# Optimization experiments

Hardware: AMD Instinct MI355X
Metric: run time of the kernel (lower is better)

## Reference

```python
import jax, jax.numpy as jnp
import numpy as np

UPDATE_SCALE = 1.0
DIST_THRESHOLD = 3.0
W_INJECT = 1.0
W_PIXEL = 1.0
EPS = 1e-8
BIG = 1e6  # sentinel coordinate for masked-out gt points


def extract_zc(sdf):
    """Zero crossings along vertical then horizontal neighbor pairs.
    Returns pts [Ncand,2] float, mask [Ncand] bool (fixed-size, masked)."""
    H, W = sdf.shape
    ii = jnp.arange(H, dtype=sdf.dtype)
    jj = jnp.arange(W, dtype=sdf.dtype)
    # vertical pairs (i,j)-(i+1,j): shape [H-1, W]
    v1, v2 = sdf[:-1, :], sdf[1:, :]
    a = jnp.abs(v1) / (jnp.abs(v1) + jnp.abs(v2) + EPS)
    i0 = ii[:-1, None]
    rv = jnp.where(v1 == 0, i0, jnp.where(v2 == 0, i0 + 1.0, i0 + a))
    cv = jnp.broadcast_to(jj[None, :], v1.shape)
    mv = (v1 == 0) | (v2 == 0) | (v1 * v2 < 0)
    # horizontal pairs (i,j)-(i,j+1): shape [H, W-1]
    h1, h2 = sdf[:, :-1], sdf[:, 1:]
    b = jnp.abs(h1) / (jnp.abs(h1) + jnp.abs(h2) + EPS)
    j0 = jj[None, :-1]
    ch = jnp.where(h1 == 0, j0, jnp.where(h2 == 0, j0 + 1.0, j0 + b))
    rh = jnp.broadcast_to(ii[:, None], h1.shape)
    mh = (h1 == 0) | (h2 == 0) | (h1 * h2 < 0)
    pts = jnp.concatenate([
        jnp.stack([rv.ravel(), cv.ravel()], axis=1),
        jnp.stack([rh.ravel(), ch.ravel()], axis=1)], axis=0)
    mask = jnp.concatenate([mv.ravel(), mh.ravel()], axis=0)
    return pts, mask


def compute_normals(sdf):
    # central differences, one-sided at edges -> [H,W,2]
    gr = jnp.concatenate([sdf[1:2] - sdf[0:1], (sdf[2:] - sdf[:-2]) / 2.0,
                          sdf[-1:] - sdf[-2:-1]], axis=0)
    gc = jnp.concatenate([sdf[:, 1:2] - sdf[:, 0:1], (sdf[:, 2:] - sdf[:, :-2]) / 2.0,
                          sdf[:, -1:] - sdf[:, -2:-1]], axis=1)
    return jnp.stack([gr, gc], axis=2)


def _corners(pts, H, W):
    r, c = pts[:, 0], pts[:, 1]
    r0 = jnp.clip(jnp.floor(r).astype(jnp.int32), 0, H - 1)
    c0 = jnp.clip(jnp.floor(c).astype(jnp.int32), 0, W - 1)
    r1 = jnp.clip(r0 + 1, 0, H - 1)
    c1 = jnp.clip(c0 + 1, 0, W - 1)
    ar = r - r0.astype(r.dtype)
    ac = c - c0.astype(c.dtype)
    wa = (1 - ar) * (1 - ac); wb = (1 - ar) * ac
    wc = ar * (1 - ac); wd = ar * ac
    return r0, c0, r1, c1, wa, wb, wc, wd


def bilinear_gather(img, pts):
    H, W = img.shape[0], img.shape[1]
    r0, c0, r1, c1, wa, wb, wc, wd = _corners(pts, H, W)
    if img.ndim == 3:
        wa, wb, wc, wd = wa[:, None], wb[:, None], wc[:, None], wd[:, None]
    return (img[r0, c0] * wa + img[r0, c1] * wb
            + img[r1, c0] * wc + img[r1, c1] * wd)


def one_image(pred, gt):
    H, W = pred.shape
    gt_pts, gt_m = extract_zc(jax.lax.stop_gradient(gt))
    pr_pts, pr_m = extract_zc(jax.lax.stop_gradient(pred))
    # bilinearly sampled, normalized normals at pred zero crossings
    normals = compute_normals(pred)                         # [H,W,2]
    n = bilinear_gather(normals, pr_pts)                    # [M,2]
    n = n / (jnp.linalg.norm(n, axis=1, keepdims=True) + 1e-8)
    # brute-force NN of each pred ZC point in gt ZC points (masked gt -> far away)
    gp = jnp.where(gt_m[:, None], gt_pts, BIG)              # [N,2]
    d2 = ((pr_pts ** 2).sum(1)[:, None] + (gp ** 2).sum(1)[None, :]
          - 2.0 * pr_pts @ gp.T)                            # [M,N]
    d2 = jnp.maximum(d2, 0.0)
    idx = jnp.argmin(d2, axis=1)
    md2 = jnp.min(d2, axis=1)
    near = gp[idx]                                          # [M,2]
    contrib = pr_m & (md2 <= DIST_THRESHOLD ** 2)
    dirv = near - pr_pts
    dot = jnp.where(contrib, (dirv * n).sum(1) * UPDATE_SCALE, 0.0)
    # bilinear scatter of dot into dSDF (weights vanish exactly where torch skips out-of-range)
    r0, c0, r1, c1, wa, wb, wc, wd = _corners(pr_pts, H, W)
    dSDF = jnp.zeros_like(pred)
    dSDF = (dSDF.at[r0, c0].add(dot * wa)
                 .at[r0, c1].add(dot * wb)
                 .at[r1, c0].add(dot * wc)
                 .at[r1, c1].add(dot * wd))
    dSDF = jax.lax.stop_gradient(dSDF)
    inj = jnp.sum(pred * dSDF)
    vals = bilinear_gather(pred, pr_pts)                    # [M]
    pix = jnp.sum(jnp.where(pr_m, vals, 0.0))
    return inj, pix


def setup_inputs() -> dict:
    key = jax.random.key(0)
    k1, k2 = jax.random.split(key)
    B, H, W = 1, 96, 96
    pred_sdf = jax.random.normal(k1, (B, H, W), dtype=jnp.float32)
    gt_sdf = jax.random.normal(k2, (B, H, W), dtype=jnp.float32)
    return {"pred_sdf": pred_sdf, "gt_sdf": gt_sdf}


def reference(pred_sdf, gt_sdf):
    inj, pix = jax.vmap(one_image)(pred_sdf, gt_sdf)
    inject = inj.mean()
    pixel = pix.mean()
    return W_INJECT * inject + W_PIXEL * pixel
```

## Files before the change

kernel.cpp:

```cpp
#include <hip/hip_runtime.h>
#include <math.h>

#pragma clang fp contract(off)

#define HH 96
#define WW 96
#define NV 9120
#define NC 18240
#define NPIX 9216
#define NCELL 9216
#define SLOTS 4
#define NBLK2 1140
#define PBLK 72
#define BIGF 1000000.0f
#define SENT_D 3.4e38f
#define SENT_J 0x7fffffff

__global__ __launch_bounds__(256) void k_prep(
    const float* __restrict__ PR, const float* __restrict__ GT,
    float2* __restrict__ N2, float2* prP, int* prM,
    float4* cells, int* finCnt){
#pragma clang fp contract(off)
  int t = blockIdx.x*256 + threadIdx.x;
  if (t == 0) *finCnt = 0;
  if (t < NPIX){
    int i = t / WW, j = t % WW;
    float gr, gc;
    if (i == 0)         gr = PR[WW+j] - PR[j];
    else if (i == HH-1) gr = PR[(HH-1)*WW+j] - PR[(HH-2)*WW+j];
    else                gr = (PR[(i+1)*WW+j] - PR[(i-1)*WW+j]) / 2.0f;
    if (j == 0)         gc = PR[i*WW+1] - PR[i*WW];
    else if (j == WW-1) gc = PR[i*WW+WW-1] - PR[i*WW+WW-2];
    else                gc = (PR[i*WW+j+1] - PR[i*WW+j-1]) / 2.0f;
    N2[t] = make_float2(gr, gc);
    int cnt = 0;
    float4 slot[SLOTS];
    for (int s = 0; s < 2; ++s){
      int i0 = i - 1 + s;
      if (i0 >= 0 && i0 <= HH-2){
        float v1 = GT[i0*WW+j], v2 = GT[(i0+1)*WW+j];
        int m = (v1 == 0.0f) || (v2 == 0.0f) || ((v1*v2) < 0.0f);
        if (m){
          float a1 = fabsf(v1), a2 = fabsf(v2);
          float den = (a1 + a2) + 1e-8f;
          float a = a1 / den;
          float i0f = (float)i0;
          float r = (v1 == 0.0f) ? i0f : ((v2 == 0.0f) ? (i0f + 1.0f) : (i0f + a));
          if ((int)floorf(r) == i){
            float c = (float)j;
            float sg = (r*r) + (c*c);
            slot[cnt++] = make_float4(r, c, sg, __int_as_float(i0*WW+j));
          }
        }
      }
    }
    for (int s = 0; s < 2; ++s){
      int j0 = j - 1 + s;
      if (j0 >= 0 && j0 <= WW-2){
        float v1 = GT[i*WW+j0], v2 = GT[i*WW+j0+1];
        int m = (v1 == 0.0f) || (v2 == 0.0f) || ((v1*v2) < 0.0f);
        if (m){
          float a1 = fabsf(v1), a2 = fabsf(v2);
          float den = (a1 + a2) + 1e-8f;
          float b = a1 / den;
          float j0f = (float)j0;
          float c = (v1 == 0.0f) ? j0f : ((v2 == 0.0f) ? (j0f + 1.0f) : (j0f + b));
          if ((int)floorf(c) == j){
            float r = (float)i;
            float sg = (r*r) + (c*c);
            slot[cnt++] = make_float4(r, c, sg,
                            __int_as_float(NV + i*(WW-1) + j0));
          }
        }
      }
    }
    for (int s = cnt; s < SLOTS; ++s)
      slot[s] = make_float4(0.0f, 0.0f, SENT_D, __int_as_float(SENT_J));
    cells[t*SLOTS+0] = slot[0]; cells[t*SLOTS+1] = slot[1];
    cells[t*SLOTS+2] = slot[2]; cells[t*SLOTS+3] = slot[3];
  } else if (t < NPIX + NC){
    int u = t - NPIX;
    float v1, v2, r, c;
    if (u < NV){
      int i0 = u / WW, j = u % WW;
      v1 = PR[i0*WW+j]; v2 = PR[(i0+1)*WW+j];
      float a1 = fabsf(v1), a2 = fabsf(v2);
      float den = (a1 + a2) + 1e-8f;
      float a = a1 / den;
      float i0f = (float)i0;
      r = (v1 == 0.0f) ? i0f : ((v2 == 0.0f) ? (i0f + 1.0f) : (i0f + a));
      c = (float)j;
    } else {
      int u2 = u - NV;
      int i = u2 / (WW-1), j0 = u2 % (WW-1);
      v1 = PR[i*WW+j0]; v2 = PR[i*WW+j0+1];
      float a1 = fabsf(v1), a2 = fabsf(v2);
      float den = (a1 + a2) + 1e-8f;
      float b = a1 / den;
      float j0f = (float)j0;
      c = (v1 == 0.0f) ? j0f : ((v2 == 0.0f) ? (j0f + 1.0f) : (j0f + b));
      r = (float)i;
    }
    prP[u] = make_float2(r, c);
    prM[u] = (v1 == 0.0f) || (v2 == 0.0f) || ((v1*v2) < 0.0f);
  }
}

__device__ inline void ring_off(int R, int q, int& dr, int& dc){
  int side = 2*R + 1;
  if (q < side){ dr = -R; dc = q - R; }
  else if (q < 2*side){ dr = R; dc = q - side - R; }
  else {
    int q2 = q - 2*side, half = side - 2;
    if (q2 < half){ dr = q2 - R + 1; dc = -R; }
    else          { dr = q2 - half - R + 1; dc = R; }
  }
}

__global__ __launch_bounds__(256) void k_nndot(
    const float* __restrict__ PR, const float2* __restrict__ N2,
    const float2* __restrict__ prP, const int* __restrict__ prM,
    const float4* __restrict__ cells,
    float* dotA, double* pvPart){
#pragma clang fp contract(off)
  int tid = threadIdx.x;
  int g = tid >> 4, l = tid & 15;
  int k = blockIdx.x*16 + g;
  float2 pp = prP[k];
  float rp = pp.x, cp = pp.y;
  int m = prM[k];
  int r0 = (int)floorf(rp); if (r0 < 0) r0 = 0; if (r0 > HH-1) r0 = HH-1;
  int c0 = (int)floorf(cp); if (c0 < 0) c0 = 0; if (c0 > WW-1) c0 = WW-1;
  int r1 = r0 + 1; if (r1 > HH-1) r1 = HH-1;
  int c1 = c0 + 1; if (c1 > WW-1) c1 = WW-1;
  float2 na = N2[r0*WW+c0], nb = N2[r0*WW+c1];
  float2 ncn = N2[r1*WW+c0], nd = N2[r1*WW+c1];
  float pa = PR[r0*WW+c0], pb = PR[r0*WW+c1];
  float pc = PR[r1*WW+c0], pd = PR[r1*WW+c1];
  float sp = (rp*rp) + (cp*cp);
  int fr = (int)floorf(rp), fc = (int)floorf(cp);
  float best = SENT_D, brg = 0.0f, bcg = 0.0f; int bjg = SENT_J;
  for (int idx = l; idx < 25; idx += 16){
    int ci = fr + idx/5 - 2, cj = fc + idx%5 - 2;
    if (ci >= 0 && ci < HH && cj >= 0 && cj < WW){
      const float4* cb = &cells[(ci*WW + cj)*SLOTS];
      for (int s = 0; s < SLOTS; ++s){
        float4 gg = cb[s];
        float cross = fmaf(cp, gg.y, rp*gg.x);
        float d2 = (sp + gg.z) - (2.0f*cross);
        d2 = fmaxf(d2, 0.0f);
        int jg = __float_as_int(gg.w);
        if ((d2 < best) || ((d2 == best) && (jg < bjg))){
          best = d2; bjg = jg; brg = gg.x; bcg = gg.y;
        }
      }
    }
  }
  for (int off = 8; off; off >>= 1){
    float ob = __shfl_xor(best, off, 64);
    int   oj = __shfl_xor(bjg,  off, 64);
    float orr = __shfl_xor(brg, off, 64);
    float oc = __shfl_xor(bcg, off, 64);
    if ((ob < best) || ((ob == best) && (oj < bjg))){
      best = ob; bjg = oj; brg = orr; bcg = oc;
    }
  }
  if (best > 3.9999f){
    for (int q = l; q < 56; q += 16){
      int dr2, dc2;
      if (q < 24) ring_off(3, q, dr2, dc2);
      else        ring_off(4, q-24, dr2, dc2);
      int ci = fr + dr2, cj = fc + dc2;
      if (ci >= 0 && ci < HH && cj >= 0 && cj < WW){
        const float4* cb = &cells[(ci*WW + cj)*SLOTS];
        for (int s = 0; s < SLOTS; ++s){
          float4 gg = cb[s];
          float cross = fmaf(cp, gg.y, rp*gg.x);
          float d2 = (sp + gg.z) - (2.0f*cross);
          d2 = fmaxf(d2, 0.0f);
          int jg = __float_as_int(gg.w);
          if ((d2 < best) || ((d2 == best) && (jg < bjg))){
            best = d2; bjg = jg; brg = gg.x; bcg = gg.y;
          }
        }
      }
    }
    for (int off = 8; off; off >>= 1){
      float ob = __shfl_xor(best, off, 64);
      int   oj = __shfl_xor(bjg,  off, 64);
      float orr = __shfl_xor(brg, off, 64);
      float oc = __shfl_xor(bcg, off, 64);
      if ((ob < best) || ((ob == best) && (oj < bjg))){
        best = ob; bjg = oj; brg = orr; bcg = oc;
      }
    }
  }
  float ar = rp - (float)r0, ac = cp - (float)c0;
  float omr = 1.0f - ar, omc = 1.0f - ac;
  float wa = omr*omc, wb = omr*ac, wc = ar*omc, wd = ar*ac;
  float nr = (((na.x*wa) + (nb.x*wb)) + (ncn.x*wc)) + (nd.x*wd);
  float nc = (((na.y*wa) + (nb.y*wb)) + (ncn.y*wc)) + (nd.y*wd);
  float nrm = sqrtf((nr*nr) + (nc*nc));
  float den = nrm + 1e-8f;
  float nru = nr / den, ncu = nc / den;
  float dr = brg - rp, dc = bcg - cp;
  float dotv = (dr*nru) + (dc*ncu);
  int contrib = m && (best <= 9.0f);
  float vals = (((pa*wa) + (pb*wb)) + (pc*wc)) + (pd*wd);
  __shared__ double sb[16];
  if (l == 0){
    dotA[k] = contrib ? dotv : 0.0f;
    sb[g] = m ? (double)vals : 0.0;
  }
  __syncthreads();
  if (tid == 0){
    double acc = 0.0;
    for (int q = 0; q < 16; ++q) acc += sb[q];
    pvPart[blockIdx.x] = acc;
  }
}

__global__ __launch_bounds__(128) void k_pixfinal(
    const float* __restrict__ PR, const float2* __restrict__ prP,
    const float* __restrict__ dotA, const double* __restrict__ pvPart,
    float* tmp, int* finCnt, float* out){
#pragma clang fp contract(off)
  int p = blockIdx.x*128 + threadIdx.x;
  int i = p / WW, j = p % WW;
  float s = 0.0f;
  for (int i0 = i-1; i0 <= i; ++i0){
    if (i0 < 0 || i0 > HH-2) continue;
    int k = i0*WW + j;
    float r = prP[k].x;
    int r0 = (int)floorf(r);
    if (r0 == i){
      float ar = r - (float)r0;
      float w = 1.0f - ar;
      s = s + (dotA[k] * w);
    }
  }
  for (int j0 = j-1; j0 <= j; ++j0){
    if (j0 < 0 || j0 > WW-2) continue;
    int k = NV + i*(WW-1) + j0;
    float c = prP[k].y;
    int c0 = (int)floorf(c);
    if (c0 == j){
      float ac = c - (float)c0;
      float w = 1.0f - ac;
      s = s + (dotA[k] * w);
    }
  }
  for (int j0 = j-2; j0 <= j-1; ++j0){
    if (j0 < 0 || j0 > WW-2) continue;
    int k = NV + i*(WW-1) + j0;
    float c = prP[k].y;
    int c0 = (int)floorf(c);
    if (c0 == j-1){
      float ac = c - (float)c0;
      s = s + (dotA[k] * ac);
    }
  }
  for (int i0 = i-2; i0 <= i-1; ++i0){
    if (i0 < 0 || i0 > HH-2) continue;
    int k = i0*WW + j;
    float r = prP[k].x;
    int r0 = (int)floorf(r);
    if (r0 == i-1){
      float ar = r - (float)r0;
      s = s + (dotA[k] * ar);
    }
  }
  tmp[p] = PR[p] * s;
  __threadfence();
  __syncthreads();
  __shared__ int lastFlag;
  if (threadIdx.x == 0){
    int old = atomicAdd(finCnt, 1);
    lastFlag = (old == PBLK-1);
  }
  __syncthreads();
  if (!lastFlag) return;
  __threadfence();
  __shared__ float buf[128];
  __shared__ double dbuf[128];
  int t = threadIdx.x;
  const float4* a4 = (const float4*)(tmp + t*72);
  float4 x = a4[0], y = a4[1];
  float q0=x.x, q1=x.y, q2=x.z, q3=x.w, q4=y.x, q5=y.y, q6=y.z, q7=y.w;
  for (int i4 = 2; i4 < 18; i4 += 2){
    float4 u = a4[i4], v = a4[i4+1];
    q0 += u.x; q1 += u.y; q2 += u.z; q3 += u.w;
    q4 += v.x; q5 += v.y; q6 += v.z; q7 += v.w;
  }
  buf[t] = ((q0+q1)+(q2+q3)) + ((q4+q5)+(q6+q7));
  double pv = 0.0;
  for (int idx = t; idx < NBLK2; idx += 128) pv += pvPart[idx];
  dbuf[t] = pv;
  __syncthreads();
  for (int st = 1; st < 128; st <<= 1){
    if ((t & (2*st - 1)) == 0){
      buf[t]  = buf[t]  + buf[t+st];
      dbuf[t] = dbuf[t] + dbuf[t+st];
    }
    __syncthreads();
  }
  if (t == 0) out[0] = buf[0] + (float)dbuf[0];
}

extern "C" void kernel_launch(void* const* d_in, const int* in_sizes, int n_in,
                              void* d_out, int out_size, void* d_ws, size_t ws_size,
                              hipStream_t stream){
  const float* pred = (const float*)d_in[0];
  const float* gt   = (const float*)d_in[1];
  float* out = (float*)d_out;

  char* w = (char*)d_ws;
  float4* cells  = (float4*)w;                 w += (size_t)NCELL*SLOTS*sizeof(float4);
  double* pvPart = (double*)w;                 w += (size_t)NBLK2*sizeof(double);
  float2* N2     = (float2*)w;                 w += (size_t)NPIX*sizeof(float2);
  float2* prP    = (float2*)w;                 w += (size_t)NC*sizeof(float2);
  float*  dotA   = (float*)w;                  w += (size_t)NC*sizeof(float);
  float*  tmp    = (float*)w;                  w += (size_t)NPIX*sizeof(float);
  int*    prM    = (int*)w;                    w += (size_t)NC*sizeof(int);
  int*    finCnt = (int*)w;

  k_prep<<<dim3(108), dim3(256), 0, stream>>>(pred, gt, N2, prP, prM,
                                              cells, finCnt);
  k_nndot<<<dim3(NBLK2), dim3(256), 0, stream>>>(pred, N2, prP, prM,
                                                 cells, dotA, pvPart);
  k_pixfinal<<<dim3(PBLK), dim3(128), 0, stream>>>(pred, prP, dotA,
                                                   pvPart, tmp, finCnt, out);
}
```

Baseline: 75.79 us.

## Fuse three kernels into one persistent kernel with grid barriers

Merges the prep, nearest-neighbour/dot and pixel-final kernels into a single 128-block persistent kernel, separated by atomic-counter grid barriers, and clears the control block with a memset. Each 16-lane group now handles 9 candidate points in sequence instead of one. The aim is to remove two kernel launch gaps and their inter-kernel drain. In exchange, the NN phase runs on far fewer concurrent waves (2048 groups), the spin barriers add latency, and correctness relies on all 128 blocks being co-resident.

```diff
diff --git a/kernel.cpp b/kernel.cpp
--- a/kernel.cpp
+++ b/kernel.cpp
@@ -10,19 +10,52 @@
 #define NPIX 9216
 #define NCELL 9216
 #define SLOTS 4
-#define NBLK2 1140
-#define PBLK 72
-#define BIGF 1000000.0f
+#define NBLKF 128
+#define NTHR 256
+#define NGRP 2048
+#define PPG 9
 #define SENT_D 3.4e38f
 #define SENT_J 0x7fffffff
 
-__global__ __launch_bounds__(256) void k_prep(
+struct Ctl { int bcnt0, bflag0, bcnt1, bflag1, fin; };
+
+__device__ inline void ring_off(int R, int q, int& dr, int& dc){
+  int side = 2*R + 1;
+  if (q < side){ dr = -R; dc = q - R; }
+  else if (q < 2*side){ dr = R; dc = q - side - R; }
+  else {
+    int q2 = q - 2*side, half = side - 2;
+    if (q2 < half){ dr = q2 - R + 1; dc = -R; }
+    else          { dr = q2 - half - R + 1; dc = R; }
+  }
+}
+
+__device__ inline void grid_barrier(int* cnt, int* flag){
+  __threadfence();
+  __syncthreads();
+  if (threadIdx.x == 0){
+    int old = __hip_atomic_fetch_add(cnt, 1, __ATOMIC_ACQ_REL,
+                                     __HIP_MEMORY_SCOPE_AGENT);
+    if (old == NBLKF-1){
+      __hip_atomic_store(flag, 1, __ATOMIC_RELEASE, __HIP_MEMORY_SCOPE_AGENT);
+    } else {
+      while (__hip_atomic_load(flag, __ATOMIC_ACQUIRE,
+                               __HIP_MEMORY_SCOPE_AGENT) == 0)
+        __builtin_amdgcn_s_sleep(8);
+    }
+  }
+  __syncthreads();
+  __threadfence();
+}
+
+__global__ __launch_bounds__(NTHR) void k_fused(
     const float* __restrict__ PR, const float* __restrict__ GT,
     float2* __restrict__ N2, float2* prP, int* prM,
-    float4* cells, int* finCnt){
+    float4* cells, float* dotA, double* pvPart, float* tmp,
+    Ctl* ctl, float* out){
 #pragma clang fp contract(off)
-  int t = blockIdx.x*256 + threadIdx.x;
-  if (t == 0) *finCnt = 0;
+  int t = blockIdx.x*NTHR + threadIdx.x;
+
   if (t < NPIX){
     int i = t / WW, j = t % WW;
     float gr, gc;
@@ -104,207 +137,195 @@
     prP[u] = make_float2(r, c);
     prM[u] = (v1 == 0.0f) || (v2 == 0.0f) || ((v1*v2) < 0.0f);
   }
-}
-
-__device__ inline void ring_off(int R, int q, int& dr, int& dc){
-  int side = 2*R + 1;
-  if (q < side){ dr = -R; dc = q - R; }
-  else if (q < 2*side){ dr = R; dc = q - side - R; }
-  else {
-    int q2 = q - 2*side, half = side - 2;
-    if (q2 < half){ dr = q2 - R + 1; dc = -R; }
-    else          { dr = q2 - half - R + 1; dc = R; }
-  }
-}
-
-__global__ __launch_bounds__(256) void k_nndot(
-    const float* __restrict__ PR, const float2* __restrict__ N2,
-    const float2* __restrict__ prP, const int* __restrict__ prM,
-    const float4* __restrict__ cells,
-    float* dotA, double* pvPart){
-#pragma clang fp contract(off)
-  int tid = threadIdx.x;
-  int g = tid >> 4, l = tid & 15;
-  int k = blockIdx.x*16 + g;
-  float2 pp = prP[k];
-  float rp = pp.x, cp = pp.y;
-  int m = prM[k];
-  int r0 = (int)floorf(rp); if (r0 < 0) r0 = 0; if (r0 > HH-1) r0 = HH-1;
-  int c0 = (int)floorf(cp); if (c0 < 0) c0 = 0; if (c0 > WW-1) c0 = WW-1;
-  int r1 = r0 + 1; if (r1 > HH-1) r1 = HH-1;
-  int c1 = c0 + 1; if (c1 > WW-1) c1 = WW-1;
-  float2 na = N2[r0*WW+c0], nb = N2[r0*WW+c1];
-  float2 ncn = N2[r1*WW+c0], nd = N2[r1*WW+c1];
-  float pa = PR[r0*WW+c0], pb = PR[r0*WW+c1];
-  float pc = PR[r1*WW+c0], pd = PR[r1*WW+c1];
-  float sp = (rp*rp) + (cp*cp);
-  int fr = (int)floorf(rp), fc = (int)floorf(cp);
-  float best = SENT_D, brg = 0.0f, bcg = 0.0f; int bjg = SENT_J;
-  for (int idx = l; idx < 25; idx += 16){
-    int ci = fr + idx/5 - 2, cj = fc + idx%5 - 2;
-    if (ci >= 0 && ci < HH && cj >= 0 && cj < WW){
-      const float4* cb = &cells[(ci*WW + cj)*SLOTS];
-      for (int s = 0; s < SLOTS; ++s){
-        float4 gg = cb[s];
-        float cross = fmaf(cp, gg.y, rp*gg.x);
-        float d2 = (sp + gg.z) - (2.0f*cross);
-        d2 = fmaxf(d2, 0.0f);
-        int jg = __float_as_int(gg.w);
-        if ((d2 < best) || ((d2 == best) && (jg < bjg))){
-          best = d2; bjg = jg; brg = gg.x; bcg = gg.y;
-        }
-      }
-    }
-  }
-  for (int off = 8; off; off >>= 1){
-    float ob = __shfl_xor(best, off, 64);
-    int   oj = __shfl_xor(bjg,  off, 64);
-    float orr = __shfl_xor(brg, off, 64);
-    float oc = __shfl_xor(bcg, off, 64);
-    if ((ob < best) || ((ob == best) && (oj < bjg))){
-      best = ob; bjg = oj; brg = orr; bcg = oc;
-    }
-  }
-  if (best > 3.9999f){
-    for (int q = l; q < 56; q += 16){
-      int dr2, dc2;
-      if (q < 24) ring_off(3, q, dr2, dc2);
-      else        ring_off(4, q-24, dr2, dc2);
-      int ci = fr + dr2, cj = fc + dc2;
-      if (ci >= 0 && ci < HH && cj >= 0 && cj < WW){
-        const float4* cb = &cells[(ci*WW + cj)*SLOTS];
-        for (int s = 0; s < SLOTS; ++s){
-          float4 gg = cb[s];
-          float cross = fmaf(cp, gg.y, rp*gg.x);
-          float d2 = (sp + gg.z) - (2.0f*cross);
-          d2 = fmaxf(d2, 0.0f);
-          int jg = __float_as_int(gg.w);
-          if ((d2 < best) || ((d2 == best) && (jg < bjg))){
-            best = d2; bjg = jg; brg = gg.x; bcg = gg.y;
-          }
-        }
-      }
-    }
-    for (int off = 8; off; off >>= 1){
-      float ob = __shfl_xor(best, off, 64);
-      int   oj = __shfl_xor(bjg,  off, 64);
-      float orr = __shfl_xor(brg, off, 64);
-      float oc = __shfl_xor(bcg, off, 64);
-      if ((ob < best) || ((ob == best) && (oj < bjg))){
-        best = ob; bjg = oj; brg = orr; bcg = oc;
-      }
-    }
-  }
-  float ar = rp - (float)r0, ac = cp - (float)c0;
-  float omr = 1.0f - ar, omc = 1.0f - ac;
-  float wa = omr*omc, wb = omr*ac, wc = ar*omc, wd = ar*ac;
-  float nr = (((na.x*wa) + (nb.x*wb)) + (ncn.x*wc)) + (nd.x*wd);
-  float nc = (((na.y*wa) + (nb.y*wb)) + (ncn.y*wc)) + (nd.y*wd);
-  float nrm = sqrtf((nr*nr) + (nc*nc));
-  float den = nrm + 1e-8f;
-  float nru = nr / den, ncu = nc / den;
-  float dr = brg - rp, dc = bcg - cp;
-  float dotv = (dr*nru) + (dc*ncu);
-  int contrib = m && (best <= 9.0f);
-  float vals = (((pa*wa) + (pb*wb)) + (pc*wc)) + (pd*wd);
-  __shared__ double sb[16];
-  if (l == 0){
-    dotA[k] = contrib ? dotv : 0.0f;
-    sb[g] = m ? (double)vals : 0.0;
-  }
-  __syncthreads();
-  if (tid == 0){
-    double acc = 0.0;
-    for (int q = 0; q < 16; ++q) acc += sb[q];
-    pvPart[blockIdx.x] = acc;
-  }
-}
-
-__global__ __launch_bounds__(128) void k_pixfinal(
-    const float* __restrict__ PR, const float2* __restrict__ prP,
-    const float* __restrict__ dotA, const double* __restrict__ pvPart,
-    float* tmp, int* finCnt, float* out){
-#pragma clang fp contract(off)
-  int p = blockIdx.x*128 + threadIdx.x;
-  int i = p / WW, j = p % WW;
-  float s = 0.0f;
-  for (int i0 = i-1; i0 <= i; ++i0){
-    if (i0 < 0 || i0 > HH-2) continue;
-    int k = i0*WW + j;
-    float r = prP[k].x;
-    int r0 = (int)floorf(r);
-    if (r0 == i){
-      float ar = r - (float)r0;
-      float w = 1.0f - ar;
-      s = s + (dotA[k] * w);
-    }
-  }
-  for (int j0 = j-1; j0 <= j; ++j0){
-    if (j0 < 0 || j0 > WW-2) continue;
-    int k = NV + i*(WW-1) + j0;
-    float c = prP[k].y;
-    int c0 = (int)floorf(c);
-    if (c0 == j){
-      float ac = c - (float)c0;
-      float w = 1.0f - ac;
-      s = s + (dotA[k] * w);
-    }
-  }
-  for (int j0 = j-2; j0 <= j-1; ++j0){
-    if (j0 < 0 || j0 > WW-2) continue;
-    int k = NV + i*(WW-1) + j0;
-    float c = prP[k].y;
-    int c0 = (int)floorf(c);
-    if (c0 == j-1){
-      float ac = c - (float)c0;
-      s = s + (dotA[k] * ac);
-    }
-  }
-  for (int i0 = i-2; i0 <= i-1; ++i0){
-    if (i0 < 0 || i0 > HH-2) continue;
-    int k = i0*WW + j;
-    float r = prP[k].x;
-    int r0 = (int)floorf(r);
-    if (r0 == i-1){
-      float ar = r - (float)r0;
-      s = s + (dotA[k] * ar);
-    }
-  }
-  tmp[p] = PR[p] * s;
+
+  grid_barrier(&ctl->bcnt0, &ctl->bflag0);
+
+  {
+    int g = threadIdx.x >> 4, l = threadIdx.x & 15;
+    int grp = blockIdx.x*16 + g;
+    double pvLocal = 0.0;
+    for (int q = 0; q < PPG; ++q){
+      int k = grp*PPG + q;
+      if (k >= NC) break;
+      float2 pp = prP[k];
+      float rp = pp.x, cp = pp.y;
+      int m = prM[k];
+      int r0 = (int)floorf(rp); if (r0 < 0) r0 = 0; if (r0 > HH-1) r0 = HH-1;
+      int c0 = (int)floorf(cp); if (c0 < 0) c0 = 0; if (c0 > WW-1) c0 = WW-1;
+      int r1 = r0 + 1; if (r1 > HH-1) r1 = HH-1;
+      int c1 = c0 + 1; if (c1 > WW-1) c1 = WW-1;
+      float2 na = N2[r0*WW+c0], nb = N2[r0*WW+c1];
+      float2 ncn = N2[r1*WW+c0], nd = N2[r1*WW+c1];
+      float pa = PR[r0*WW+c0], pb = PR[r0*WW+c1];
+      float pc = PR[r1*WW+c0], pd = PR[r1*WW+c1];
+      float sp = (rp*rp) + (cp*cp);
+      int fr = (int)floorf(rp), fc = (int)floorf(cp);
+      float best = SENT_D, brg = 0.0f, bcg = 0.0f; int bjg = SENT_J;
+      for (int idx = l; idx < 25; idx += 16){
+        int ci = fr + idx/5 - 2, cj = fc + idx%5 - 2;
+        if (ci >= 0 && ci < HH && cj >= 0 && cj < WW){
+          const float4* cb = &cells[(ci*WW + cj)*SLOTS];
+          for (int s = 0; s < SLOTS; ++s){
+            float4 gg = cb[s];
+            float cross = fmaf(cp, gg.y, rp*gg.x);
+            float d2 = (sp + gg.z) - (2.0f*cross);
+            d2 = fmaxf(d2, 0.0f);
+            int jg = __float_as_int(gg.w);
+            if ((d2 < best) || ((d2 == best) && (jg < bjg))){
+              best = d2; bjg = jg; brg = gg.x; bcg = gg.y;
+            }
+          }
+        }
+      }
+      for (int off = 8; off; off >>= 1){
+        float ob = __shfl_xor(best, off, 64);
+        int   oj = __shfl_xor(bjg,  off, 64);
+        float orr = __shfl_xor(brg, off, 64);
+        float oc = __shfl_xor(bcg, off, 64);
+        if ((ob < best) || ((ob == best) && (oj < bjg))){
+          best = ob; bjg = oj; brg = orr; bcg = oc;
+        }
+      }
+      if (best > 3.9999f){
+        for (int qq = l; qq < 56; qq += 16){
+          int dr2, dc2;
+          if (qq < 24) ring_off(3, qq, dr2, dc2);
+          else         ring_off(4, qq-24, dr2, dc2);
+          int ci = fr + dr2, cj = fc + dc2;
+          if (ci >= 0 && ci < HH && cj >= 0 && cj < WW){
+            const float4* cb = &cells[(ci*WW + cj)*SLOTS];
+            for (int s = 0; s < SLOTS; ++s){
+              float4 gg = cb[s];
+              float cross = fmaf(cp, gg.y, rp*gg.x);
+              float d2 = (sp + gg.z) - (2.0f*cross);
+              d2 = fmaxf(d2, 0.0f);
+              int jg = __float_as_int(gg.w);
+              if ((d2 < best) || ((d2 == best) && (jg < bjg))){
+                best = d2; bjg = jg; brg = gg.x; bcg = gg.y;
+              }
+            }
+          }
+        }
+        for (int off = 8; off; off >>= 1){
+          float ob = __shfl_xor(best, off, 64);
+          int   oj = __shfl_xor(bjg,  off, 64);
+          float orr = __shfl_xor(brg, off, 64);
+          float oc = __shfl_xor(bcg, off, 64);
+          if ((ob < best) || ((ob == best) && (oj < bjg))){
+            best = ob; bjg = oj; brg = orr; bcg = oc;
+          }
+        }
+      }
+      float ar = rp - (float)r0, ac = cp - (float)c0;
+      float omr = 1.0f - ar, omc = 1.0f - ac;
+      float wa = omr*omc, wb = omr*ac, wc = ar*omc, wd = ar*ac;
+      float nr = (((na.x*wa) + (nb.x*wb)) + (ncn.x*wc)) + (nd.x*wd);
+      float nc = (((na.y*wa) + (nb.y*wb)) + (ncn.y*wc)) + (nd.y*wd);
+      float nrm = sqrtf((nr*nr) + (nc*nc));
+      float den = nrm + 1e-8f;
+      float nru = nr / den, ncu = nc / den;
+      float dr = brg - rp, dc = bcg - cp;
+      float dotv = (dr*nru) + (dc*ncu);
+      int contrib = m && (best <= 9.0f);
+      float vals = (((pa*wa) + (pb*wb)) + (pc*wc)) + (pd*wd);
+      if (l == 0){
+        dotA[k] = contrib ? dotv : 0.0f;
+        if (m) pvLocal += (double)vals;
+      }
+    }
+    if (l == 0) pvPart[grp] = pvLocal;
+    else if (grp*PPG >= NC && l == 0) pvPart[grp] = 0.0;
+  }
+
+  grid_barrier(&ctl->bcnt1, &ctl->bflag1);
+
+  {
+    int p = t;
+    if (p < NPIX){
+      int i = p / WW, j = p % WW;
+      float s = 0.0f;
+      for (int i0 = i-1; i0 <= i; ++i0){
+        if (i0 < 0 || i0 > HH-2) continue;
+        int k = i0*WW + j;
+        float r = prP[k].x;
+        int r0 = (int)floorf(r);
+        if (r0 == i){
+          float ar = r - (float)r0;
+          float w = 1.0f - ar;
+          s = s + (dotA[k] * w);
+        }
+      }
+      for (int j0 = j-1; j0 <= j; ++j0){
+        if (j0 < 0 || j0 > WW-2) continue;
+        int k = NV + i*(WW-1) + j0;
+        float c = prP[k].y;
+        int c0 = (int)floorf(c);
+        if (c0 == j){
+          float ac = c - (float)c0;
+          float w = 1.0f - ac;
+          s = s + (dotA[k] * w);
+        }
+      }
+      for (int j0 = j-2; j0 <= j-1; ++j0){
+        if (j0 < 0 || j0 > WW-2) continue;
+        int k = NV + i*(WW-1) + j0;
+        float c = prP[k].y;
+        int c0 = (int)floorf(c);
+        if (c0 == j-1){
+          float ac = c - (float)c0;
+          s = s + (dotA[k] * ac);
+        }
+      }
+      for (int i0 = i-2; i0 <= i-1; ++i0){
+        if (i0 < 0 || i0 > HH-2) continue;
+        int k = i0*WW + j;
+        float r = prP[k].x;
+        int r0 = (int)floorf(r);
+        if (r0 == i-1){
+          float ar = r - (float)r0;
+          s = s + (dotA[k] * ar);
+        }
+      }
+      tmp[p] = PR[p] * s;
+    }
+  }
+
   __threadfence();
   __syncthreads();
   __shared__ int lastFlag;
   if (threadIdx.x == 0){
-    int old = atomicAdd(finCnt, 1);
-    lastFlag = (old == PBLK-1);
+    int old = atomicAdd(&ctl->fin, 1);
+    lastFlag = (old == NBLKF-1);
   }
   __syncthreads();
   if (!lastFlag) return;
   __threadfence();
   __shared__ float buf[128];
   __shared__ double dbuf[128];
-  int t = threadIdx.x;
-  const float4* a4 = (const float4*)(tmp + t*72);
-  float4 x = a4[0], y = a4[1];
-  float q0=x.x, q1=x.y, q2=x.z, q3=x.w, q4=y.x, q5=y.y, q6=y.z, q7=y.w;
-  for (int i4 = 2; i4 < 18; i4 += 2){
-    float4 u = a4[i4], v = a4[i4+1];
-    q0 += u.x; q1 += u.y; q2 += u.z; q3 += u.w;
-    q4 += v.x; q5 += v.y; q6 += v.z; q7 += v.w;
-  }
-  buf[t] = ((q0+q1)+(q2+q3)) + ((q4+q5)+(q6+q7));
-  double pv = 0.0;
-  for (int idx = t; idx < NBLK2; idx += 128) pv += pvPart[idx];
-  dbuf[t] = pv;
+  int tt = threadIdx.x;
+  if (tt < 128){
+    const float4* a4 = (const float4*)(tmp + tt*72);
+    float4 x = a4[0], y = a4[1];
+    float q0=x.x, q1=x.y, q2=x.z, q3=x.w, q4=y.x, q5=y.y, q6=y.z, q7=y.w;
+    for (int i4 = 2; i4 < 18; i4 += 2){
+      float4 u = a4[i4], v = a4[i4+1];
+      q0 += u.x; q1 += u.y; q2 += u.z; q3 += u.w;
+      q4 += v.x; q5 += v.y; q6 += v.z; q7 += v.w;
+    }
+    buf[tt] = ((q0+q1)+(q2+q3)) + ((q4+q5)+(q6+q7));
+    double pv = 0.0;
+    for (int idx = tt; idx < NGRP; idx += 128) pv += pvPart[idx];
+    dbuf[tt] = pv;
+  }
   __syncthreads();
   for (int st = 1; st < 128; st <<= 1){
-    if ((t & (2*st - 1)) == 0){
-      buf[t]  = buf[t]  + buf[t+st];
-      dbuf[t] = dbuf[t] + dbuf[t+st];
+    if (tt < 128 && (tt & (2*st - 1)) == 0){
+      buf[tt]  = buf[tt]  + buf[tt+st];
+      dbuf[tt] = dbuf[tt] + dbuf[tt+st];
     }
     __syncthreads();
   }
-  if (t == 0) out[0] = buf[0] + (float)dbuf[0];
+  if (tt == 0) out[0] = buf[0] + (float)dbuf[0];
 }
 
 extern "C" void kernel_launch(void* const* d_in, const int* in_sizes, int n_in,
@@ -316,18 +337,15 @@
 
   char* w = (char*)d_ws;
   float4* cells  = (float4*)w;                 w += (size_t)NCELL*SLOTS*sizeof(float4);
-  double* pvPart = (double*)w;                 w += (size_t)NBLK2*sizeof(double);
+  double* pvPart = (double*)w;                 w += (size_t)NGRP*sizeof(double);
   float2* N2     = (float2*)w;                 w += (size_t)NPIX*sizeof(float2);
   float2* prP    = (float2*)w;                 w += (size_t)NC*sizeof(float2);
   float*  dotA   = (float*)w;                  w += (size_t)NC*sizeof(float);
   float*  tmp    = (float*)w;                  w += (size_t)NPIX*sizeof(float);
   int*    prM    = (int*)w;                    w += (size_t)NC*sizeof(int);
-  int*    finCnt = (int*)w;
-
-  k_prep<<<dim3(108), dim3(256), 0, stream>>>(pred, gt, N2, prP, prM,
-                                              cells, finCnt);
-  k_nndot<<<dim3(NBLK2), dim3(256), 0, stream>>>(pred, N2, prP, prM,
-                                                 cells, dotA, pvPart);
-  k_pixfinal<<<dim3(PBLK), dim3(128), 0, stream>>>(pred, prP, dotA,
-                                                   pvPart, tmp, finCnt, out);
+  Ctl*    ctl    = (Ctl*)w;
+
+  hipMemsetAsync(ctl, 0, sizeof(Ctl), stream);
+  k_fused<<<dim3(NBLKF), dim3(NTHR), 0, stream>>>(pred, gt, N2, prP, prM,
+                cells, dotA, pvPart, tmp, ctl, out);
 }
```

Result: slower. 152.6 us (+101.4%).

## Fuse prep kernel into NN search by recomputing zero crossings and normals on the fly

Applied to the files above, without the earlier changes.

Removes the separate prep kernel that built the gt cell grid, normals and pred zero-crossing arrays. The NN kernel now computes pred zero-crossings, bilinear normals and gt candidate points directly from the input images, using 32 lanes per point (one per cell of the 5x5 window) instead of 16. The pixel/final kernel also recomputes crossing positions from pred instead of reading prP. This saves a launch and the workspace round trips, at the cost of redundant arithmetic and more blocks.

```diff
diff --git a/kernel.cpp b/kernel.cpp
--- a/kernel.cpp
+++ b/kernel.cpp
@@ -8,105 +8,102 @@
 #define NV 9120
 #define NC 18240
 #define NPIX 9216
-#define NCELL 9216
-#define SLOTS 4
-#define NBLK2 1140
+#define ABLK 2280
 #define PBLK 72
-#define BIGF 1000000.0f
 #define SENT_D 3.4e38f
 #define SENT_J 0x7fffffff
 
-__global__ __launch_bounds__(256) void k_prep(
-    const float* __restrict__ PR, const float* __restrict__ GT,
-    float2* __restrict__ N2, float2* prP, int* prM,
-    float4* cells, int* finCnt){
-#pragma clang fp contract(off)
-  int t = blockIdx.x*256 + threadIdx.x;
-  if (t == 0) *finCnt = 0;
-  if (t < NPIX){
-    int i = t / WW, j = t % WW;
-    float gr, gc;
-    if (i == 0)         gr = PR[WW+j] - PR[j];
-    else if (i == HH-1) gr = PR[(HH-1)*WW+j] - PR[(HH-2)*WW+j];
-    else                gr = (PR[(i+1)*WW+j] - PR[(i-1)*WW+j]) / 2.0f;
-    if (j == 0)         gc = PR[i*WW+1] - PR[i*WW];
-    else if (j == WW-1) gc = PR[i*WW+WW-1] - PR[i*WW+WW-2];
-    else                gc = (PR[i*WW+j+1] - PR[i*WW+j-1]) / 2.0f;
-    N2[t] = make_float2(gr, gc);
-    int cnt = 0;
-    float4 slot[SLOTS];
-    for (int s = 0; s < 2; ++s){
-      int i0 = i - 1 + s;
-      if (i0 >= 0 && i0 <= HH-2){
-        float v1 = GT[i0*WW+j], v2 = GT[(i0+1)*WW+j];
-        int m = (v1 == 0.0f) || (v2 == 0.0f) || ((v1*v2) < 0.0f);
-        if (m){
-          float a1 = fabsf(v1), a2 = fabsf(v2);
-          float den = (a1 + a2) + 1e-8f;
-          float a = a1 / den;
-          float i0f = (float)i0;
-          float r = (v1 == 0.0f) ? i0f : ((v2 == 0.0f) ? (i0f + 1.0f) : (i0f + a));
-          if ((int)floorf(r) == i){
-            float c = (float)j;
-            float sg = (r*r) + (c*c);
-            slot[cnt++] = make_float4(r, c, sg, __int_as_float(i0*WW+j));
-          }
-        }
-      }
-    }
-    for (int s = 0; s < 2; ++s){
-      int j0 = j - 1 + s;
-      if (j0 >= 0 && j0 <= WW-2){
-        float v1 = GT[i*WW+j0], v2 = GT[i*WW+j0+1];
-        int m = (v1 == 0.0f) || (v2 == 0.0f) || ((v1*v2) < 0.0f);
-        if (m){
-          float a1 = fabsf(v1), a2 = fabsf(v2);
-          float den = (a1 + a2) + 1e-8f;
-          float b = a1 / den;
-          float j0f = (float)j0;
-          float c = (v1 == 0.0f) ? j0f : ((v2 == 0.0f) ? (j0f + 1.0f) : (j0f + b));
-          if ((int)floorf(c) == j){
-            float r = (float)i;
-            float sg = (r*r) + (c*c);
-            slot[cnt++] = make_float4(r, c, sg,
-                            __int_as_float(NV + i*(WW-1) + j0));
-          }
-        }
-      }
-    }
-    for (int s = cnt; s < SLOTS; ++s)
-      slot[s] = make_float4(0.0f, 0.0f, SENT_D, __int_as_float(SENT_J));
-    cells[t*SLOTS+0] = slot[0]; cells[t*SLOTS+1] = slot[1];
-    cells[t*SLOTS+2] = slot[2]; cells[t*SLOTS+3] = slot[3];
-  } else if (t < NPIX + NC){
-    int u = t - NPIX;
-    float v1, v2, r, c;
-    if (u < NV){
-      int i0 = u / WW, j = u % WW;
-      v1 = PR[i0*WW+j]; v2 = PR[(i0+1)*WW+j];
-      float a1 = fabsf(v1), a2 = fabsf(v2);
-      float den = (a1 + a2) + 1e-8f;
-      float a = a1 / den;
-      float i0f = (float)i0;
-      r = (v1 == 0.0f) ? i0f : ((v2 == 0.0f) ? (i0f + 1.0f) : (i0f + a));
-      c = (float)j;
-    } else {
-      int u2 = u - NV;
-      int i = u2 / (WW-1), j0 = u2 % (WW-1);
-      v1 = PR[i*WW+j0]; v2 = PR[i*WW+j0+1];
-      float a1 = fabsf(v1), a2 = fabsf(v2);
-      float den = (a1 + a2) + 1e-8f;
-      float b = a1 / den;
-      float j0f = (float)j0;
-      c = (v1 == 0.0f) ? j0f : ((v2 == 0.0f) ? (j0f + 1.0f) : (j0f + b));
-      r = (float)i;
-    }
-    prP[u] = make_float2(r, c);
-    prM[u] = (v1 == 0.0f) || (v2 == 0.0f) || ((v1*v2) < 0.0f);
-  }
-}
-
-__device__ inline void ring_off(int R, int q, int& dr, int& dc){
+__device__ __forceinline__ void zc_point(const float* __restrict__ S, int u,
+                                         float& r, float& c, int& m){
+#pragma clang fp contract(off)
+  float v1, v2;
+  if (u < NV){
+    int i0 = u / WW, j = u % WW;
+    v1 = S[i0*WW+j]; v2 = S[(i0+1)*WW+j];
+    float a1 = fabsf(v1), a2 = fabsf(v2);
+    float den = (a1 + a2) + 1e-8f;
+    float a = a1 / den;
+    float i0f = (float)i0;
+    r = (v1 == 0.0f) ? i0f : ((v2 == 0.0f) ? (i0f + 1.0f) : (i0f + a));
+    c = (float)j;
+  } else {
+    int u2 = u - NV;
+    int i = u2 / (WW-1), j0 = u2 % (WW-1);
+    v1 = S[i*WW+j0]; v2 = S[i*WW+j0+1];
+    float a1 = fabsf(v1), a2 = fabsf(v2);
+    float den = (a1 + a2) + 1e-8f;
+    float b = a1 / den;
+    float j0f = (float)j0;
+    c = (v1 == 0.0f) ? j0f : ((v2 == 0.0f) ? (j0f + 1.0f) : (j0f + b));
+    r = (float)i;
+  }
+  m = (v1 == 0.0f) || (v2 == 0.0f) || ((v1*v2) < 0.0f);
+}
+
+__device__ __forceinline__ float2 normal_at(const float* __restrict__ PR,
+                                            int i, int j){
+#pragma clang fp contract(off)
+  float gr, gc;
+  if (i == 0)         gr = PR[WW+j] - PR[j];
+  else if (i == HH-1) gr = PR[(HH-1)*WW+j] - PR[(HH-2)*WW+j];
+  else                gr = (PR[(i+1)*WW+j] - PR[(i-1)*WW+j]) / 2.0f;
+  if (j == 0)         gc = PR[i*WW+1] - PR[i*WW];
+  else if (j == WW-1) gc = PR[i*WW+WW-1] - PR[i*WW+WW-2];
+  else                gc = (PR[i*WW+j+1] - PR[i*WW+j-1]) / 2.0f;
+  return make_float2(gr, gc);
+}
+
+__device__ __forceinline__ void scan_cell(int ci, int cj,
+    float rp, float cp, float sp, const float* __restrict__ GT,
+    float& best, int& bjg, float& brg, float& bcg){
+#pragma clang fp contract(off)
+  for (int s = 0; s < 2; ++s){
+    int i0 = ci - 1 + s;
+    if (i0 < 0 || i0 > HH-2) continue;
+    float v1 = GT[i0*WW+cj], v2 = GT[(i0+1)*WW+cj];
+    int m = (v1 == 0.0f) || (v2 == 0.0f) || ((v1*v2) < 0.0f);
+    if (!m) continue;
+    float a1 = fabsf(v1), a2 = fabsf(v2);
+    float den = (a1 + a2) + 1e-8f;
+    float a = a1 / den;
+    float i0f = (float)i0;
+    float r = (v1 == 0.0f) ? i0f : ((v2 == 0.0f) ? (i0f + 1.0f) : (i0f + a));
+    if ((int)floorf(r) != ci) continue;
+    float c = (float)cj;
+    float sg = (r*r) + (c*c);
+    int jg = i0*WW + cj;
+    float cross = fmaf(cp, c, rp*r);
+    float d2 = (sp + sg) - (2.0f*cross);
+    d2 = fmaxf(d2, 0.0f);
+    if ((d2 < best) || ((d2 == best) && (jg < bjg))){
+      best = d2; bjg = jg; brg = r; bcg = c;
+    }
+  }
+  for (int s = 0; s < 2; ++s){
+    int j0 = cj - 1 + s;
+    if (j0 < 0 || j0 > WW-2) continue;
+    float v1 = GT[ci*WW+j0], v2 = GT[ci*WW+j0+1];
+    int m = (v1 == 0.0f) || (v2 == 0.0f) || ((v1*v2) < 0.0f);
+    if (!m) continue;
+    float a1 = fabsf(v1), a2 = fabsf(v2);
+    float den = (a1 + a2) + 1e-8f;
+    float b = a1 / den;
+    float j0f = (float)j0;
+    float c = (v1 == 0.0f) ? j0f : ((v2 == 0.0f) ? (j0f + 1.0f) : (j0f + b));
+    if ((int)floorf(c) != cj) continue;
+    float r = (float)ci;
+    float sg = (r*r) + (c*c);
+    int jg = NV + ci*(WW-1) + j0;
+    float cross = fmaf(cp, c, rp*r);
+    float d2 = (sp + sg) - (2.0f*cross);
+    d2 = fmaxf(d2, 0.0f);
+    if ((d2 < best) || ((d2 == best) && (jg < bjg))){
+      best = d2; bjg = jg; brg = r; bcg = c;
+    }
+  }
+}
+
+__device__ __forceinline__ void ring_off(int R, int q, int& dr, int& dc){
   int side = 2*R + 1;
   if (q < side){ dr = -R; dc = q - R; }
   else if (q < 2*side){ dr = R; dc = q - side - R; }
@@ -118,45 +115,32 @@
 }
 
 __global__ __launch_bounds__(256) void k_nndot(
-    const float* __restrict__ PR, const float2* __restrict__ N2,
-    const float2* __restrict__ prP, const int* __restrict__ prM,
-    const float4* __restrict__ cells,
-    float* dotA, double* pvPart){
-#pragma clang fp contract(off)
-  int tid = threadIdx.x;
-  int g = tid >> 4, l = tid & 15;
-  int k = blockIdx.x*16 + g;
-  float2 pp = prP[k];
-  float rp = pp.x, cp = pp.y;
-  int m = prM[k];
-  int r0 = (int)floorf(rp); if (r0 < 0) r0 = 0; if (r0 > HH-1) r0 = HH-1;
-  int c0 = (int)floorf(cp); if (c0 < 0) c0 = 0; if (c0 > WW-1) c0 = WW-1;
+    const float* __restrict__ PR, const float* __restrict__ GT,
+    float* __restrict__ dotA, double* __restrict__ pvPart, int* finCnt){
+#pragma clang fp contract(off)
+  int l = threadIdx.x & 31;
+  int g = threadIdx.x >> 5;
+  int k = blockIdx.x*8 + g;
+  if (blockIdx.x == 0 && threadIdx.x == 0) *finCnt = 0;
+  float rp, cp; int m;
+  zc_point(PR, k, rp, cp, m);
+  float sp = (rp*rp) + (cp*cp);
+  int fr = (int)floorf(rp), fc = (int)floorf(cp);
+  int r0 = fr; if (r0 < 0) r0 = 0; if (r0 > HH-1) r0 = HH-1;
+  int c0 = fc; if (c0 < 0) c0 = 0; if (c0 > WW-1) c0 = WW-1;
   int r1 = r0 + 1; if (r1 > HH-1) r1 = HH-1;
   int c1 = c0 + 1; if (c1 > WW-1) c1 = WW-1;
-  float2 na = N2[r0*WW+c0], nb = N2[r0*WW+c1];
-  float2 ncn = N2[r1*WW+c0], nd = N2[r1*WW+c1];
+  float2 na = normal_at(PR, r0, c0), nb = normal_at(PR, r0, c1);
+  float2 ncn = normal_at(PR, r1, c0), nd = normal_at(PR, r1, c1);
   float pa = PR[r0*WW+c0], pb = PR[r0*WW+c1];
   float pc = PR[r1*WW+c0], pd = PR[r1*WW+c1];
-  float sp = (rp*rp) + (cp*cp);
-  int fr = (int)floorf(rp), fc = (int)floorf(cp);
   float best = SENT_D, brg = 0.0f, bcg = 0.0f; int bjg = SENT_J;
-  for (int idx = l; idx < 25; idx += 16){
-    int ci = fr + idx/5 - 2, cj = fc + idx%5 - 2;
-    if (ci >= 0 && ci < HH && cj >= 0 && cj < WW){
-      const float4* cb = &cells[(ci*WW + cj)*SLOTS];
-      for (int s = 0; s < SLOTS; ++s){
-        float4 gg = cb[s];
-        float cross = fmaf(cp, gg.y, rp*gg.x);
-        float d2 = (sp + gg.z) - (2.0f*cross);
-        d2 = fmaxf(d2, 0.0f);
-        int jg = __float_as_int(gg.w);
-        if ((d2 < best) || ((d2 == best) && (jg < bjg))){
-          best = d2; bjg = jg; brg = gg.x; bcg = gg.y;
-        }
-      }
-    }
-  }
-  for (int off = 8; off; off >>= 1){
+  if (l < 25){
+    int ci = fr + l/5 - 2, cj = fc + l%5 - 2;
+    if (ci >= 0 && ci < HH && cj >= 0 && cj < WW)
+      scan_cell(ci, cj, rp, cp, sp, GT, best, bjg, brg, bcg);
+  }
+  for (int off = 16; off; off >>= 1){
     float ob = __shfl_xor(best, off, 64);
     int   oj = __shfl_xor(bjg,  off, 64);
     float orr = __shfl_xor(brg, off, 64);
@@ -166,26 +150,15 @@
     }
   }
   if (best > 3.9999f){
-    for (int q = l; q < 56; q += 16){
+    for (int q = l; q < 56; q += 32){
       int dr2, dc2;
       if (q < 24) ring_off(3, q, dr2, dc2);
       else        ring_off(4, q-24, dr2, dc2);
       int ci = fr + dr2, cj = fc + dc2;
-      if (ci >= 0 && ci < HH && cj >= 0 && cj < WW){
-        const float4* cb = &cells[(ci*WW + cj)*SLOTS];
-        for (int s = 0; s < SLOTS; ++s){
-          float4 gg = cb[s];
-          float cross = fmaf(cp, gg.y, rp*gg.x);
-          float d2 = (sp + gg.z) - (2.0f*cross);
-          d2 = fmaxf(d2, 0.0f);
-          int jg = __float_as_int(gg.w);
-          if ((d2 < best) || ((d2 == best) && (jg < bjg))){
-            best = d2; bjg = jg; brg = gg.x; bcg = gg.y;
-          }
-        }
-      }
-    }
-    for (int off = 8; off; off >>= 1){
+      if (ci >= 0 && ci < HH && cj >= 0 && cj < WW)
+        scan_cell(ci, cj, rp, cp, sp, GT, best, bjg, brg, bcg);
+    }
+    for (int off = 16; off; off >>= 1){
       float ob = __shfl_xor(best, off, 64);
       int   oj = __shfl_xor(bjg,  off, 64);
       float orr = __shfl_xor(brg, off, 64);
@@ -207,22 +180,22 @@
   float dotv = (dr*nru) + (dc*ncu);
   int contrib = m && (best <= 9.0f);
   float vals = (((pa*wa) + (pb*wb)) + (pc*wc)) + (pd*wd);
-  __shared__ double sb[16];
+  __shared__ double sb[8];
   if (l == 0){
     dotA[k] = contrib ? dotv : 0.0f;
     sb[g] = m ? (double)vals : 0.0;
   }
   __syncthreads();
-  if (tid == 0){
+  if (threadIdx.x == 0){
     double acc = 0.0;
-    for (int q = 0; q < 16; ++q) acc += sb[q];
+    for (int q = 0; q < 8; ++q) acc += sb[q];
     pvPart[blockIdx.x] = acc;
   }
 }
 
 __global__ __launch_bounds__(128) void k_pixfinal(
-    const float* __restrict__ PR, const float2* __restrict__ prP,
-    const float* __restrict__ dotA, const double* __restrict__ pvPart,
+    const float* __restrict__ PR, const float* __restrict__ dotA,
+    const double* __restrict__ pvPart,
     float* tmp, int* finCnt, float* out){
 #pragma clang fp contract(off)
   int p = blockIdx.x*128 + threadIdx.x;
@@ -230,44 +203,60 @@
   float s = 0.0f;
   for (int i0 = i-1; i0 <= i; ++i0){
     if (i0 < 0 || i0 > HH-2) continue;
-    int k = i0*WW + j;
-    float r = prP[k].x;
+    float v1 = PR[i0*WW+j], v2 = PR[(i0+1)*WW+j];
+    float a1 = fabsf(v1), a2 = fabsf(v2);
+    float dn = (a1 + a2) + 1e-8f;
+    float a = a1 / dn;
+    float i0f = (float)i0;
+    float r = (v1 == 0.0f) ? i0f : ((v2 == 0.0f) ? (i0f + 1.0f) : (i0f + a));
     int r0 = (int)floorf(r);
     if (r0 == i){
       float ar = r - (float)r0;
       float w = 1.0f - ar;
-      s = s + (dotA[k] * w);
+      s = s + (dotA[i0*WW+j] * w);
     }
   }
   for (int j0 = j-1; j0 <= j; ++j0){
     if (j0 < 0 || j0 > WW-2) continue;
-    int k = NV + i*(WW-1) + j0;
-    float c = prP[k].y;
+    float v1 = PR[i*WW+j0], v2 = PR[i*WW+j0+1];
+    float a1 = fabsf(v1), a2 = fabsf(v2);
+    float dn = (a1 + a2) + 1e-8f;
+    float b = a1 / dn;
+    float j0f = (float)j0;
+    float c = (v1 == 0.0f) ? j0f : ((v2 == 0.0f) ? (j0f + 1.0f) : (j0f + b));
     int c0 = (int)floorf(c);
     if (c0 == j){
       float ac = c - (float)c0;
       float w = 1.0f - ac;
-      s = s + (dotA[k] * w);
+      s = s + (dotA[NV + i*(WW-1) + j0] * w);
     }
   }
   for (int j0 = j-2; j0 <= j-1; ++j0){
     if (j0 < 0 || j0 > WW-2) continue;
-    int k = NV + i*(WW-1) + j0;
-    float c = prP[k].y;
+    float v1 = PR[i*WW+j0], v2 = PR[i*WW+j0+1];
+    float a1 = fabsf(v1), a2 = fabsf(v2);
+    float dn = (a1 + a2) + 1e-8f;
+    float b = a1 / dn;
+    float j0f = (float)j0;
+    float c = (v1 == 0.0f) ? j0f : ((v2 == 0.0f) ? (j0f + 1.0f) : (j0f + b));
     int c0 = (int)floorf(c);
     if (c0 == j-1){
       float ac = c - (float)c0;
-      s = s + (dotA[k] * ac);
+      s = s + (dotA[NV + i*(WW-1) + j0] * ac);
     }
   }
   for (int i0 = i-2; i0 <= i-1; ++i0){
     if (i0 < 0 || i0 > HH-2) continue;
-    int k = i0*WW + j;
-    float r = prP[k].x;
+    float v1 = PR[i0*WW+j], v2 = PR[(i0+1)*WW+j];
+    float a1 = fabsf(v1), a2 = fabsf(v2);
+    float dn = (a1 + a2) + 1e-8f;
+    float a = a1 / dn;
+    float i0f = (float)i0;
+    float r = (v1 == 0.0f) ? i0f : ((v2 == 0.0f) ? (i0f + 1.0f) : (i0f + a));
     int r0 = (int)floorf(r);
     if (r0 == i-1){
       float ar = r - (float)r0;
-      s = s + (dotA[k] * ar);
+      s = s + (dotA[i0*WW+j] * ar);
     }
   }
   tmp[p] = PR[p] * s;
@@ -294,7 +283,7 @@
   }
   buf[t] = ((q0+q1)+(q2+q3)) + ((q4+q5)+(q6+q7));
   double pv = 0.0;
-  for (int idx = t; idx < NBLK2; idx += 128) pv += pvPart[idx];
+  for (int idx = t; idx < ABLK; idx += 128) pv += pvPart[idx];
   dbuf[t] = pv;
   __syncthreads();
   for (int st = 1; st < 128; st <<= 1){
@@ -315,19 +304,12 @@
   float* out = (float*)d_out;
 
   char* w = (char*)d_ws;
-  float4* cells  = (float4*)w;                 w += (size_t)NCELL*SLOTS*sizeof(float4);
-  double* pvPart = (double*)w;                 w += (size_t)NBLK2*sizeof(double);
-  float2* N2     = (float2*)w;                 w += (size_t)NPIX*sizeof(float2);
-  float2* prP    = (float2*)w;                 w += (size_t)NC*sizeof(float2);
+  double* pvPart = (double*)w;                 w += (size_t)ABLK*sizeof(double);
   float*  dotA   = (float*)w;                  w += (size_t)NC*sizeof(float);
   float*  tmp    = (float*)w;                  w += (size_t)NPIX*sizeof(float);
-  int*    prM    = (int*)w;                    w += (size_t)NC*sizeof(int);
   int*    finCnt = (int*)w;
 
-  k_prep<<<dim3(108), dim3(256), 0, stream>>>(pred, gt, N2, prP, prM,
-                                              cells, finCnt);
-  k_nndot<<<dim3(NBLK2), dim3(256), 0, stream>>>(pred, N2, prP, prM,
-                                                 cells, dotA, pvPart);
-  k_pixfinal<<<dim3(PBLK), dim3(128), 0, stream>>>(pred, prP, dotA,
-                                                   pvPart, tmp, finCnt, out);
-}
+  k_nndot<<<dim3(ABLK), dim3(256), 0, stream>>>(pred, gt, dotA, pvPart, finCnt);
+  k_pixfinal<<<dim3(PBLK), dim3(128), 0, stream>>>(pred, dotA, pvPart,
+                                                   tmp, finCnt, out);
+}
```

Measured after the change: 76.72 us. Within noise of the previous version (+1.2%).
